# Kernel tuning notes

Measured on AMD Instinct MI355X. Metric: run time of the kernel, lower is better.

## Reference

```python
import jax, jax.numpy as jnp
import numpy as np

B, S = 1, 1536
D_MODEL, NHEAD, HEAD_DIM = 1024, 16, 64
ROPE, NUM_SEQ = 32, 4
KVC, QC, D_FF = 256, 384, 4096
SPP = S // NUM_SEQ                      # seq per stock = 384
EPS_RMS = 1.1920929e-07                 # torch RMSNorm default eps = finfo(fp32).eps
ATTN_EPS = 1e-5
LAMBDA_INIT = 0.8 - 0.6 * float(np.exp(-0.3 * 0.0))  # depth 0 -> 0.2
SCALING = float(((HEAD_DIM + ROPE) // 2) ** -0.5)


def rmsnorm(x, w, eps=EPS_RMS):
    var = jnp.mean(jnp.square(x), axis=-1, keepdims=True)
    return x * jax.lax.rsqrt(var + eps) * w


def setup_inputs() -> dict:
    key = jax.random.key(0)
    ks = jax.random.split(key, 16)
    sd = 0.02
    inv_freq = 1.0 / (10000.0 ** (np.arange(0, ROPE // 4) / (ROPE // 4)))
    ang = np.arange(1, SPP)[:, None] * inv_freq[None, :]  # [SPP-1, ROPE//4]
    return {
        "x": jax.random.normal(ks[0], (B, S, D_MODEL), jnp.float32),
        "freqs_cos": jnp.asarray(np.cos(ang), jnp.float32),
        "freqs_sin": jnp.asarray(np.sin(ang), jnp.float32),
        "norm1_w": jnp.ones((D_MODEL,), jnp.float32),
        "norm2_w": jnp.ones((D_MODEL,), jnp.float32),
        "kv_down_w": jax.random.normal(ks[1], (KVC + ROPE, D_MODEL), jnp.float32) * sd,
        "q_down_w": jax.random.normal(ks[2], (QC, D_MODEL), jnp.float32) * sd,
        "kv_norm_w": jnp.ones((KVC,), jnp.float32),
        "q_norm_w": jnp.ones((QC,), jnp.float32),
        "kv_up_w": jax.random.normal(ks[3], (HEAD_DIM * NHEAD * 2, KVC), jnp.float32) * sd,
        "q_up_w": jax.random.normal(ks[4], ((HEAD_DIM + ROPE) * NHEAD, QC), jnp.float32) * sd,
        "lambda_q1": jax.random.normal(ks[5], (HEAD_DIM // 2,), jnp.float32) * 0.1,
        "lambda_k1": jax.random.normal(ks[6], (HEAD_DIM // 2,), jnp.float32) * 0.1,
        "lambda_q2": jax.random.normal(ks[7], (HEAD_DIM // 2,), jnp.float32) * 0.1,
        "lambda_k2": jax.random.normal(ks[8], (HEAD_DIM // 2,), jnp.float32) * 0.1,
        "attn_norm_w": jnp.ones((HEAD_DIM,), jnp.float32),
        "o_w": jax.random.normal(ks[9], (D_MODEL, NHEAD * HEAD_DIM), jnp.float32) * sd,
        "ff_in_w": jax.random.normal(ks[10], (D_FF * 2, D_MODEL), jnp.float32) * sd,
        "ff_out_w": jax.random.normal(ks[11], (D_MODEL, D_FF), jnp.float32) * sd,
    }


def reference(x, freqs_cos, freqs_sin, norm1_w, norm2_w, kv_down_w, q_down_w,
              kv_norm_w, q_norm_w, kv_up_w, q_up_w, lambda_q1, lambda_k1,
              lambda_q2, lambda_k2, attn_norm_w, o_w, ff_in_w, ff_out_w):
    b, s, _ = x.shape
    spp = s // NUM_SEQ
    H2, hd2 = 2 * NHEAD, HEAD_DIM // 2

    # block-tiled causal mask (1 = masked), matching mask.repeat(..., num_seq, num_seq)
    base = jnp.triu(jnp.ones((spp, spp), jnp.float32), 1)
    mask = jnp.tile(base, (NUM_SEQ, NUM_SEQ))  # [S, S]

    xin = rmsnorm(x, norm1_w)
    ckv = xin @ kv_down_w.T                                    # [B,S,KVC+ROPE]
    c_kv, k_rope = ckv[..., :KVC], ckv[..., KVC:]
    kv = (rmsnorm(c_kv, kv_norm_w) @ kv_up_w.T).reshape(b, s, NHEAD, 2 * HEAD_DIM)
    k, v = kv[..., :HEAD_DIM], kv[..., HEAD_DIM:]
    k = k.reshape(b, s, H2, hd2)
    qf = (rmsnorm(xin @ q_down_w.T, q_norm_w) @ q_up_w.T).reshape(b, s, NHEAD, HEAD_DIM + ROPE)
    q, q_rope = qf[..., :HEAD_DIM], qf[..., HEAD_DIM:]
    q = q.reshape(b, s, H2, hd2)
    k_rope = jnp.tile(k_rope[:, :, None, :], (1, 1, NHEAD, 1)).reshape(b, s, H2, ROPE // 2)
    q_rope = q_rope.reshape(b, s, H2, ROPE // 2)

    # rotary emb; position 0 of every ticker is left untouched (identity rotation)
    cos = jnp.concatenate([jnp.ones((1, ROPE // 4), freqs_cos.dtype), freqs_cos], 0)  # [spp, ROPE//4]
    sin = jnp.concatenate([jnp.zeros((1, ROPE // 4), freqs_sin.dtype), freqs_sin], 0)

    def rot(r):
        # S is laid out as (position, ticker) interleaved: s = p*NUM_SEQ + t
        r = r.reshape(b, spp, NUM_SEQ, H2, ROPE // 4, 2)
        c = cos[None, :, None, None, :]
        s_ = sin[None, :, None, None, :]
        r0, r1 = r[..., 0], r[..., 1]
        y = jnp.stack([r0 * c - r1 * s_, r0 * s_ + r1 * c], axis=-1)
        return y.reshape(b, s, H2, ROPE // 2)

    q = jnp.concatenate([q, rot(q_rope)], -1).transpose(0, 2, 1, 3)  # [B,2H,S,dk]
    k = jnp.concatenate([k, rot(k_rope)], -1).transpose(0, 2, 1, 3)
    v = v.transpose(0, 2, 1, 3)                                      # [B,H,S,hd]

    a = jnp.einsum('bhqd,bhkd->bhqk', q, k) * SCALING
    a = jnp.where(mask[None, None] == 1, -1e9, a)
    a = jax.nn.softmax(a, axis=-1)

    lam = jnp.exp(jnp.sum(lambda_k1 * lambda_q1)) - jnp.exp(jnp.sum(lambda_k2 * lambda_q2)) + LAMBDA_INIT
    a = a.reshape(b, NHEAD, 2, s, s)
    a1, a2 = a[:, :, 0], a[:, :, 1]
    g = jnp.mean(a1, axis=-2, keepdims=True)            # [B,H,1,S], broadcasts over queries
    a = a1 - lam * a2 + lam * g
    a = jnp.where(mask[None, None] == 1, 0.0, a)

    out = jnp.einsum('bhqk,bhkd->bhqd', a, v)           # [B,H,S,hd]
    out = rmsnorm(out.transpose(0, 2, 1, 3), attn_norm_w, eps=ATTN_EPS).transpose(0, 2, 1, 3)
    # faithful to source: raw reshape of [B,H,S,hd] -> [B,S,H*hd] (transposes cancel)
    out = out.reshape(b, s, NHEAD * HEAD_DIM)
    x = x + out @ o_w.T

    h = rmsnorm(x, norm2_w)
    uv = h @ ff_in_w.T
    u, vg = uv[..., :D_FF], uv[..., D_FF:]
    return x + (u * jax.nn.silu(vg)) @ ff_out_w.T
```

## Files before the change

kernel.cpp:

```cpp
#include <hip/hip_runtime.h>
#include <math.h>

#define S     1536
#define DM    1024
#define NH    16
#define H2N   32
#define HD    64
#define KVC   256
#define QC    384
#define DFF   4096
#define SPP   384
#define DQK   48
#define EPS_RMS  1.1920929e-07f
#define ATTN_EPS 1e-5f
#define SCALING  0.14433756729740643f

typedef float f32x4 __attribute__((ext_vector_type(4)));
typedef float f32x16 __attribute__((ext_vector_type(16)));
typedef short bf16x8 __attribute__((ext_vector_type(8)));

__device__ __forceinline__ short cvt_bf16(float f) {
  union { float f; unsigned u; } x; x.f = f;
  unsigned r = x.u + 0x7FFFu + ((x.u >> 16) & 1u);
  return (short)(r >> 16);
}
__device__ __forceinline__ unsigned pk2(float a, float b) {
  unsigned r;
  asm("v_cvt_pk_bf16_f32 %0, %1, %2" : "=v"(r) : "v"(a), "v"(b));
  return r;
}
__device__ __forceinline__ bf16x8 cvt8(float4 a, float4 b) {
  union { unsigned u[4]; bf16x8 v; } r;
  r.u[0] = pk2(a.x, a.y); r.u[1] = pk2(a.z, a.w);
  r.u[2] = pk2(b.x, b.y); r.u[3] = pk2(b.z, b.w);
  return r.v;
}

__global__ __launch_bounds__(256) void cvt_w4(const float* __restrict__ s0, int n0,
    const float* __restrict__ s1, int n1, const float* __restrict__ s2, int n2,
    const float* __restrict__ s3, int n3, short* __restrict__ dst) {
  long base = (long)blockIdx.x * 2048 + (long)threadIdx.x * 8;
  const float* src; long off;
  if (base < n0) { src = s0; off = base; }
  else if (base < (long)n0 + n1) { src = s1; off = base - n0; }
  else if (base < (long)n0 + n1 + n2) { src = s2; off = base - n0 - n1; }
  else { src = s3; off = base - n0 - n1 - n2; }
  float4 a = *reinterpret_cast<const float4*>(src + off);
  float4 b = *reinterpret_cast<const float4*>(src + off + 4);
  *reinterpret_cast<bf16x8*>(dst + base) = cvt8(a, b);
}

__global__ __launch_bounds__(256) void rmsnorm_bf(const float* __restrict__ in,
    const float* __restrict__ w, short* __restrict__ out,
    int cols, int ldin, int ldout, float eps) {
  const int row = blockIdx.x;
  const float* xr = in + (size_t)row * ldin;
  short* yr = out + (size_t)row * ldout;
  const int tid = threadIdx.x;
  float ss = 0.f;
  for (int c = tid << 2; c < cols; c += 1024) {
    float4 v = *reinterpret_cast<const float4*>(xr + c);
    ss += v.x*v.x + v.y*v.y + v.z*v.z + v.w*v.w;
  }
#pragma unroll
  for (int mm = 1; mm < 64; mm <<= 1) ss += __shfl_xor(ss, mm, 64);
  __shared__ float red[4];
  if ((tid & 63) == 0) red[tid >> 6] = ss;
  __syncthreads();
  float tot = red[0] + red[1] + red[2] + red[3];
  float scale = rsqrtf(tot / (float)cols + eps);
  for (int c = tid << 2; c < cols; c += 1024) {
    float4 v = *reinterpret_cast<const float4*>(xr + c);
    float4 wv = *reinterpret_cast<const float4*>(w + c);
    uint2 p;
    p.x = pk2(v.x*scale*wv.x, v.y*scale*wv.y);
    p.y = pk2(v.z*scale*wv.z, v.w*scale*wv.w);
    *reinterpret_cast<uint2*>(yr + c) = p;
  }
}

__global__ __launch_bounds__(256) void rmsnorm_sum_bf(const float* __restrict__ p0,
    const float* __restrict__ p1, const float* __restrict__ xres,
    const float* __restrict__ w, float* __restrict__ outw, short* __restrict__ yb,
    float eps) {
  const int row = blockIdx.x;
  const int c = threadIdx.x << 2;
  const size_t base = (size_t)row * DM + c;
  float4 a = *reinterpret_cast<const float4*>(p0 + base);
  float4 b = *reinterpret_cast<const float4*>(p1 + base);
  float4 xv = *reinterpret_cast<const float4*>(xres + base);
  float4 v = make_float4(a.x+b.x+xv.x, a.y+b.y+xv.y, a.z+b.z+xv.z, a.w+b.w+xv.w);
  *reinterpret_cast<float4*>(outw + base) = v;
  float ss = v.x*v.x + v.y*v.y + v.z*v.z + v.w*v.w;
#pragma unroll
  for (int mm = 1; mm < 64; mm <<= 1) ss += __shfl_xor(ss, mm, 64);
  __shared__ float red[4];
  if ((threadIdx.x & 63) == 0) red[threadIdx.x >> 6] = ss;
  __syncthreads();
  float tot = red[0] + red[1] + red[2] + red[3];
  float scale = rsqrtf(tot * (1.0f / (float)DM) + eps);
  float4 wv = *reinterpret_cast<const float4*>(w + c);
  uint2 p;
  p.x = pk2(v.x*scale*wv.x, v.y*scale*wv.y);
  p.y = pk2(v.z*scale*wv.z, v.w*scale*wv.w);
  *reinterpret_cast<uint2*>(yb + base) = p;
}

__global__ __launch_bounds__(256) void fadd2(float* __restrict__ out,
    const float* __restrict__ p0, const float* __restrict__ p1) {
  size_t i = ((size_t)blockIdx.x * 256 + threadIdx.x) << 2;
  float4 o = *reinterpret_cast<float4*>(out + i);
  float4 a = *reinterpret_cast<const float4*>(p0 + i);
  float4 b = *reinterpret_cast<const float4*>(p1 + i);
  o.x += a.x + b.x; o.y += a.y + b.y; o.z += a.z + b.z; o.w += a.w + b.w;
  *reinterpret_cast<float4*>(out + i) = o;
}

template<int ADD>
__global__ __launch_bounds__(256) void mgemm_nt(const short* __restrict__ A,
    const short* __restrict__ B, const float* __restrict__ src, float* __restrict__ C,
    int M, int N, int K, int lda, int ldb, int ldc) {
  __shared__ short As[64][72];
  __shared__ short Bs[64][72];
  const int bm = blockIdx.y * 64, bn = blockIdx.x * 64;
  const int tid = threadIdx.x;
  const int w = tid >> 6, lane = tid & 63;
  const int wr = (w >> 1) << 5, wc = (w & 1) << 5;
  const int srow = tid >> 2, sk = (tid & 3) << 4;
  const int lrow = lane & 15, lk8 = (lane >> 4) << 3;
  const int arow = bm + srow, brow = bn + srow;
  const bool bvalid = brow < N;
  f32x4 acc[2][2];
#pragma unroll
  for (int i = 0; i < 2; ++i)
#pragma unroll
    for (int j = 0; j < 2; ++j) acc[i][j] = (f32x4){0.f, 0.f, 0.f, 0.f};

  bf16x8 rah0, rah1, rbh0, rbh1;
  {
    const short* ap = A + (size_t)arow * lda + sk;
    rah0 = *reinterpret_cast<const bf16x8*>(ap);
    rah1 = *reinterpret_cast<const bf16x8*>(ap + 8);
  }
  rbh0 = (bf16x8){0,0,0,0,0,0,0,0}; rbh1 = rbh0;
  if (bvalid) {
    const short* bp = B + (size_t)brow * ldb + sk;
    rbh0 = *reinterpret_cast<const bf16x8*>(bp);
    rbh1 = *reinterpret_cast<const bf16x8*>(bp + 8);
  }

  for (int k0 = 0; k0 < K; k0 += 64) {
    bf16x8 va0 = rah0, va1 = rah1, vb0 = rbh0, vb1 = rbh1;
    __syncthreads();
    *reinterpret_cast<bf16x8*>(&As[srow][sk])     = va0;
    *reinterpret_cast<bf16x8*>(&As[srow][sk + 8]) = va1;
    *reinterpret_cast<bf16x8*>(&Bs[srow][sk])     = vb0;
    *reinterpret_cast<bf16x8*>(&Bs[srow][sk + 8]) = vb1;
    __syncthreads();
    const int kn = k0 + 64;
    if (kn < K) {
      const short* ap = A + (size_t)arow * lda + kn + sk;
      rah0 = *reinterpret_cast<const bf16x8*>(ap);
      rah1 = *reinterpret_cast<const bf16x8*>(ap + 8);
      if (bvalid) {
        const short* bp = B + (size_t)brow * ldb + kn + sk;
        rbh0 = *reinterpret_cast<const bf16x8*>(bp);
        rbh1 = *reinterpret_cast<const bf16x8*>(bp + 8);
      }
    }
#pragma unroll
    for (int kk = 0; kk < 2; ++kk) {
      bf16x8 af0 = *reinterpret_cast<bf16x8*>(&As[wr + lrow][(kk << 5) + lk8]);
      bf16x8 af1 = *reinterpret_cast<bf16x8*>(&As[wr + 16 + lrow][(kk << 5) + lk8]);
      bf16x8 bf0 = *reinterpret_cast<bf16x8*>(&Bs[wc + lrow][(kk << 5) + lk8]);
      bf16x8 bf1 = *reinterpret_cast<bf16x8*>(&Bs[wc + 16 + lrow][(kk << 5) + lk8]);
      acc[0][0] = __builtin_amdgcn_mfma_f32_16x16x32_bf16(af0, bf0, acc[0][0], 0, 0, 0);
      acc[0][1] = __builtin_amdgcn_mfma_f32_16x16x32_bf16(af0, bf1, acc[0][1], 0, 0, 0);
      acc[1][0] = __builtin_amdgcn_mfma_f32_16x16x32_bf16(af1, bf0, acc[1][0], 0, 0, 0);
      acc[1][1] = __builtin_amdgcn_mfma_f32_16x16x32_bf16(af1, bf1, acc[1][1], 0, 0, 0);
    }
  }
  const int crow0 = bm + wr + ((lane >> 4) << 2);
  const int ccol0 = bn + wc + lrow;
#pragma unroll
  for (int mi = 0; mi < 2; ++mi)
#pragma unroll
    for (int ni = 0; ni < 2; ++ni) {
      int colc = ccol0 + (ni << 4);
      if (colc < N) {
#pragma unroll
        for (int r = 0; r < 4; ++r) {
          int rowc = crow0 + (mi << 4) + r;
          float v = acc[mi][ni][r];
          if (ADD) v += src[(size_t)rowc * ldc + colc];
          C[(size_t)rowc * ldc + colc] = v;
        }
      }
    }
}

__global__ __launch_bounds__(256) void mgemm_sk(const short* __restrict__ A,
    const short* __restrict__ B, float* __restrict__ P0, float* __restrict__ P1,
    int M, int N, int K2, int lda, int ldb, int ldc) {
  __shared__ short As[64][72];
  __shared__ short Bs[64][72];
  const int bm = blockIdx.y * 64, bn = blockIdx.x * 64;
  const int koff = blockIdx.z * K2;
  float* C = blockIdx.z ? P1 : P0;
  const int tid = threadIdx.x;
  const int w = tid >> 6, lane = tid & 63;
  const int wr = (w >> 1) << 5, wc = (w & 1) << 5;
  const int srow = tid >> 2, sk = (tid & 3) << 4;
  const int lrow = lane & 15, lk8 = (lane >> 4) << 3;
  const int arow = bm + srow, brow = bn + srow;
  f32x4 acc[2][2];
#pragma unroll
  for (int i = 0; i < 2; ++i)
#pragma unroll
    for (int j = 0; j < 2; ++j) acc[i][j] = (f32x4){0.f, 0.f, 0.f, 0.f};

  bf16x8 rah0, rah1, rbh0, rbh1;
  {
    const short* ap = A + (size_t)arow * lda + koff + sk;
    rah0 = *reinterpret_cast<const bf16x8*>(ap);
    rah1 = *reinterpret_cast<const bf16x8*>(ap + 8);
    const short* bp = B + (size_t)brow * ldb + koff + sk;
    rbh0 = *reinterpret_cast<const bf16x8*>(bp);
    rbh1 = *reinterpret_cast<const bf16x8*>(bp + 8);
  }
  const int kend = koff + K2;
  for (int k0 = koff; k0 < kend; k0 += 64) {
    bf16x8 va0 = rah0, va1 = rah1, vb0 = rbh0, vb1 = rbh1;
    __syncthreads();
    *reinterpret_cast<bf16x8*>(&As[srow][sk])     = va0;
    *reinterpret_cast<bf16x8*>(&As[srow][sk + 8]) = va1;
    *reinterpret_cast<bf16x8*>(&Bs[srow][sk])     = vb0;
    *reinterpret_cast<bf16x8*>(&Bs[srow][sk + 8]) = vb1;
    __syncthreads();
    const int kn = k0 + 64;
    if (kn < kend) {
      const short* ap = A + (size_t)arow * lda + kn + sk;
      rah0 = *reinterpret_cast<const bf16x8*>(ap);
      rah1 = *reinterpret_cast<const bf16x8*>(ap + 8);
      const short* bp = B + (size_t)brow * ldb + kn + sk;
      rbh0 = *reinterpret_cast<const bf16x8*>(bp);
      rbh1 = *reinterpret_cast<const bf16x8*>(bp + 8);
    }
#pragma unroll
    for (int kk = 0; kk < 2; ++kk) {
      bf16x8 af0 = *reinterpret_cast<bf16x8*>(&As[wr + lrow][(kk << 5) + lk8]);
      bf16x8 af1 = *reinterpret_cast<bf16x8*>(&As[wr + 16 + lrow][(kk << 5) + lk8]);
      bf16x8 bf0 = *reinterpret_cast<bf16x8*>(&Bs[wc + lrow][(kk << 5) + lk8]);
      bf16x8 bf1 = *reinterpret_cast<bf16x8*>(&Bs[wc + 16 + lrow][(kk << 5) + lk8]);
      acc[0][0] = __builtin_amdgcn_mfma_f32_16x16x32_bf16(af0, bf0, acc[0][0], 0, 0, 0);
      acc[0][1] = __builtin_amdgcn_mfma_f32_16x16x32_bf16(af0, bf1, acc[0][1], 0, 0, 0);
      acc[1][0] = __builtin_amdgcn_mfma_f32_16x16x32_bf16(af1, bf0, acc[1][0], 0, 0, 0);
      acc[1][1] = __builtin_amdgcn_mfma_f32_16x16x32_bf16(af1, bf1, acc[1][1], 0, 0, 0);
    }
  }
  const int crow0 = bm + wr + ((lane >> 4) << 2);
  const int ccol0 = bn + wc + lrow;
#pragma unroll
  for (int mi = 0; mi < 2; ++mi)
#pragma unroll
    for (int ni = 0; ni < 2; ++ni) {
      int colc = ccol0 + (ni << 4);
#pragma unroll
      for (int r = 0; r < 4; ++r) {
        int rowc = crow0 + (mi << 4) + r;
        C[(size_t)rowc * ldc + colc] = acc[mi][ni][r];
      }
    }
}

__global__ __launch_bounds__(256) void mgemm_glu(const short* __restrict__ A,
    const short* __restrict__ Bw, short* __restrict__ C,
    int M, int N, int K, int lda, int ldb, int ldc) {
  __shared__ short As[128][72];
  __shared__ short Bu[64][72];
  __shared__ short Bv[64][72];
  const int bm = blockIdx.y * 128, bn = blockIdx.x * 64;
  const int tid = threadIdx.x;
  const int w = tid >> 6, lane = tid & 63;
  const int wr = (w >> 1) << 6, wc = (w & 1) << 5;
  const int arow = bm + (tid >> 1), ac = (tid & 1) << 5;
  const int brow = bn + (tid >> 2), bc = (tid & 3) << 4;
  const int lrow = lane & 15, lk8 = (lane >> 4) << 3;
  f32x4 au[4][2], av[4][2];
#pragma unroll
  for (int i = 0; i < 4; ++i)
#pragma unroll
    for (int j = 0; j < 2; ++j) {
      au[i][j] = (f32x4){0.f, 0.f, 0.f, 0.f};
      av[i][j] = (f32x4){0.f, 0.f, 0.f, 0.f};
    }
  bf16x8 ra[4], ru[2], rv[2];
  {
    const short* ap = A + (size_t)arow * lda + ac;
    const short* up = Bw + (size_t)brow * ldb + bc;
    const short* vp = Bw + (size_t)(N + brow) * ldb + bc;
#pragma unroll
    for (int e = 0; e < 4; ++e) ra[e] = *reinterpret_cast<const bf16x8*>(ap + (e << 3));
    ru[0] = *reinterpret_cast<const bf16x8*>(up);
    ru[1] = *reinterpret_cast<const bf16x8*>(up + 8);
    rv[0] = *reinterpret_cast<const bf16x8*>(vp);
    rv[1] = *reinterpret_cast<const bf16x8*>(vp + 8);
  }
  for (int k0 = 0; k0 < K; k0 += 64) {
    __syncthreads();
#pragma unroll
    for (int e = 0; e < 4; ++e)
      *reinterpret_cast<bf16x8*>(&As[tid >> 1][ac + (e << 3)]) = ra[e];
    *reinterpret_cast<bf16x8*>(&Bu[tid >> 2][bc])     = ru[0];
    *reinterpret_cast<bf16x8*>(&Bu[tid >> 2][bc + 8]) = ru[1];
    *reinterpret_cast<bf16x8*>(&Bv[tid >> 2][bc])     = rv[0];
    *reinterpret_cast<bf16x8*>(&Bv[tid >> 2][bc + 8]) = rv[1];
    __syncthreads();
    const int kn = k0 + 64;
    if (kn < K) {
      const short* ap = A + (size_t)arow * lda + kn + ac;
      const short* up = Bw + (size_t)brow * ldb + kn + bc;
      const short* vp = Bw + (size_t)(N + brow) * ldb + kn + bc;
#pragma unroll
      for (int e = 0; e < 4; ++e) ra[e] = *reinterpret_cast<const bf16x8*>(ap + (e << 3));
      ru[0] = *reinterpret_cast<const bf16x8*>(up);
      ru[1] = *reinterpret_cast<const bf16x8*>(up + 8);
      rv[0] = *reinterpret_cast<const bf16x8*>(vp);
      rv[1] = *reinterpret_cast<const bf16x8*>(vp + 8);
    }
#pragma unroll
    for (int kk = 0; kk < 2; ++kk) {
      bf16x8 af[4], uf[2], vf[2];
#pragma unroll
      for (int i = 0; i < 4; ++i)
        af[i] = *reinterpret_cast<bf16x8*>(&As[wr + (i << 4) + lrow][(kk << 5) + lk8]);
#pragma unroll
      for (int j = 0; j < 2; ++j) {
        uf[j] = *reinterpret_cast<bf16x8*>(&Bu[wc + (j << 4) + lrow][(kk << 5) + lk8]);
        vf[j] = *reinterpret_cast<bf16x8*>(&Bv[wc + (j << 4) + lrow][(kk << 5) + lk8]);
      }
#pragma unroll
      for (int i = 0; i < 4; ++i)
#pragma unroll
        for (int j = 0; j < 2; ++j) {
          au[i][j] = __builtin_amdgcn_mfma_f32_16x16x32_bf16(af[i], uf[j], au[i][j], 0, 0, 0);
          av[i][j] = __builtin_amdgcn_mfma_f32_16x16x32_bf16(af[i], vf[j], av[i][j], 0, 0, 0);
        }
    }
  }
  const int crow0 = bm + wr + ((lane >> 4) << 2);
  const int ccol0 = bn + wc + lrow;
#pragma unroll
  for (int mi = 0; mi < 4; ++mi)
#pragma unroll
    for (int ni = 0; ni < 2; ++ni) {
      int colc = ccol0 + (ni << 4);
#pragma unroll
      for (int r = 0; r < 4; ++r) {
        int rowc = crow0 + (mi << 4) + r;
        float uu = au[mi][ni][r], vg = av[mi][ni][r];
        float sig = 1.0f / (1.0f + __expf(-vg));
        C[(size_t)rowc * ldc + colc] = cvt_bf16(uu * vg * sig);
      }
    }
}

__global__ __launch_bounds__(256) void build_qk(const float* __restrict__ qf,
    const float* __restrict__ kvb, const float* __restrict__ ckv,
    const float* __restrict__ fc, const float* __restrict__ fs,
    short* __restrict__ Qb, short* __restrict__ Kb) {
  int t = blockIdx.x * 256 + threadIdx.x;
  int h2 = blockIdx.y;
  if (t >= S) return;
  int hh = h2 >> 1, par = h2 & 1;
  const float* qrow = qf + (size_t)t*1536 + hh*96;
  const float* krow = kvb + (size_t)t*2048 + hh*128;
  unsigned qu[24], ku[24];
#pragma unroll
  for (int xq = 0; xq < 8; ++xq) {
    float4 qv = *reinterpret_cast<const float4*>(qrow + par*32 + (xq<<2));
    float4 kv = *reinterpret_cast<const float4*>(krow + par*32 + (xq<<2));
    qu[xq*2]   = pk2(qv.x, qv.y); qu[xq*2+1] = pk2(qv.z, qv.w);
    ku[xq*2]   = pk2(kv.x, kv.y); ku[xq*2+1] = pk2(kv.z, kv.w);
  }
  int p = t >> 2;
  const float* qr = qrow + 64 + par*16;
  const float* kr = ckv + (size_t)t*288 + 256 + par*16;
#pragma unroll
  for (int mq = 0; mq < 8; ++mq) {
    float c = 1.f, sn = 0.f;
    if (p > 0) { c = fc[(p-1)*8 + mq]; sn = fs[(p-1)*8 + mq]; }
    float q0 = qr[2*mq], q1 = qr[2*mq+1];
    qu[16 + mq] = pk2(q0*c - q1*sn, q0*sn + q1*c);
    float k0 = kr[2*mq], k1 = kr[2*mq+1];
    ku[16 + mq] = pk2(k0*c - k1*sn, k0*sn + k1*c);
  }
  unsigned* qo = (unsigned*)(Qb + ((size_t)h2*S + t)*DQK);
  unsigned* ko = (unsigned*)(Kb + ((size_t)h2*S + t)*DQK);
#pragma unroll
  for (int e = 0; e < 6; ++e) {
    *reinterpret_cast<uint4*>(qo + (e<<2)) = make_uint4(qu[e*4], qu[e*4+1], qu[e*4+2], qu[e*4+3]);
    *reinterpret_cast<uint4*>(ko + (e<<2)) = make_uint4(ku[e*4], ku[e*4+1], ku[e*4+2], ku[e*4+3]);
  }
}

__global__ __launch_bounds__(256) void vt_build(const float* __restrict__ kvb,
    short* __restrict__ Vt) {
  const int hh = blockIdx.x;
  const int t0 = blockIdx.y << 7;
  __shared__ short Ts[128][74];
  const int tl = threadIdx.x >> 3, dp = (threadIdx.x & 7) << 3;
#pragma unroll
  for (int pass = 0; pass < 4; ++pass) {
    int t = t0 + (pass << 5) + tl;
    const float* vp = kvb + (size_t)t*2048 + hh*128 + 64 + dp;
    float4 a = *reinterpret_cast<const float4*>(vp);
    float4 b = *reinterpret_cast<const float4*>(vp + 4);
    *reinterpret_cast<bf16x8*>(&Ts[(pass << 5) + tl][dp]) = cvt8(a, b);
  }
  __syncthreads();
  for (int idx = threadIdx.x; idx < 1024; idx += 256) {
    int d = idx >> 4, tseg = (idx & 15) << 3;
    bf16x8 v;
#pragma unroll
    for (int e = 0; e < 8; ++e) v[e] = Ts[tseg + e][d];
    *reinterpret_cast<bf16x8*>(Vt + ((size_t)hh*HD + d)*S + t0 + tseg) = v;
  }
}

__global__ void compute_lam(const float* __restrict__ lq1, const float* __restrict__ lk1,
                            const float* __restrict__ lq2, const float* __restrict__ lk2,
                            float* __restrict__ lamp) {
  int t = threadIdx.x;
  float a = lq1[t]*lk1[t];
  float b = lq2[t]*lk2[t];
#pragma unroll
  for (int mm = 1; mm < 32; mm <<= 1) { a += __shfl_xor(a, mm, 32); b += __shfl_xor(b, mm, 32); }
  if (t == 0) lamp[0] = expf(a) - expf(b) + 0.2f;
}

__global__ __launch_bounds__(256) void flash_mfma(const short* __restrict__ Qb,
    const short* __restrict__ Kb, const short* __restrict__ Vg,
    float* __restrict__ Ob, float* __restrict__ rowm, float* __restrict__ rowl,
    float* __restrict__ Ob1a, float* __restrict__ Ob1b,
    float* __restrict__ rm1, float* __restrict__ rl1) {
  const int h2 = blockIdx.y;
  const int hh = h2 >> 1;
  const int z  = blockIdx.z;
  const int tid = threadIdx.x;
  const int w = tid >> 6, lane = tid & 63;
  const int ql = lane & 31, h = lane >> 5;
  const int cq = blockIdx.x / 3, k = blockIdx.x % 3;
  const int qi = k + 3*w;
  const int qbase = cq*SPP + (qi << 5);
  const int ri0w = qi << 5;

  __shared__ __align__(16) float Ot[4][32][36];

  bf16x8 qf0, qf1, qf2;
  {
    const short* qp = Qb + ((size_t)h2*S + qbase + ql)*DQK + (h << 3);
    qf0 = *reinterpret_cast<const bf16x8*>(qp);
    qf1 = *reinterpret_cast<const bf16x8*>(qp + 16);
    qf2 = *reinterpret_cast<const bf16x8*>(qp + 32);
  }
  const short* Kbase = Kb + (size_t)h2*S*DQK + (h << 3);
  const short* V0 = Vg + ((size_t)hh*HD + ql)*S + (h << 3);
  const short* V1 = Vg + ((size_t)hh*HD + 32 + ql)*S + (h << 3);

  float m = -1e30f, l = 0.f;
  f32x16 o0, o1;
#pragma unroll
  for (int r = 0; r < 16; ++r) { o0[r] = 0.f; o1[r] = 0.f; }

  for (int c = (z << 1); c < (z << 1) + 2; ++c) {
    for (int jr = 0; jr <= ri0w; jr += 32) {
      const int j0 = c*SPP + jr;
      const bool diag = (jr == ri0w);
      const short* kp = Kbase + (size_t)(j0 + ql)*DQK;
      bf16x8 kf0 = *reinterpret_cast<const bf16x8*>(kp);
      bf16x8 kf1 = *reinterpret_cast<const bf16x8*>(kp + 16);
      bf16x8 kf2 = *reinterpret_cast<const bf16x8*>(kp + 32);
      bf16x8 v00 = *reinterpret_cast<const bf16x8*>(V0 + j0);
      bf16x8 v01 = *reinterpret_cast<const bf16x8*>(V0 + j0 + 16);
      bf16x8 v10 = *reinterpret_cast<const bf16x8*>(V1 + j0);
      bf16x8 v11 = *reinterpret_cast<const bf16x8*>(V1 + j0 + 16);

      f32x16 st;
#pragma unroll
      for (int r = 0; r < 16; ++r) st[r] = 0.f;
      st = __builtin_amdgcn_mfma_f32_32x32x16_bf16(kf0, qf0, st, 0, 0, 0);
      st = __builtin_amdgcn_mfma_f32_32x32x16_bf16(kf1, qf1, st, 0, 0, 0);
      st = __builtin_amdgcn_mfma_f32_32x32x16_bf16(kf2, qf2, st, 0, 0, 0);

      if (diag) {
#pragma unroll
        for (int r = 0; r < 16; ++r) {
          int kl = (r & 3) + ((r >> 2) << 3) + (h << 2);
          st[r] = (kl <= ql) ? st[r] * SCALING : -1e30f;
        }
      } else {
#pragma unroll
        for (int r = 0; r < 16; ++r) st[r] *= SCALING;
      }

      float tm = st[0];
#pragma unroll
      for (int r = 1; r < 16; ++r) tm = fmaxf(tm, st[r]);
      tm = fmaxf(tm, __shfl_xor(tm, 32));
      if (__any(tm > m + 8.0f)) {
        float mnew = fmaxf(m, tm);
        float sc = __expf(m - mnew);
        m = mnew;
        l *= sc;
#pragma unroll
        for (int r = 0; r < 16; ++r) { o0[r] *= sc; o1[r] *= sc; }
      }
      float ps = 0.f;
#pragma unroll
      for (int r = 0; r < 16; ++r) { float p = __expf(st[r] - m); st[r] = p; ps += p; }
      ps += __shfl_xor(ps, 32);
      l += ps;

      unsigned A0 = pk2(st[0],  st[1]),  B0 = pk2(st[2],  st[3]);
      unsigned C0 = pk2(st[4],  st[5]),  D0 = pk2(st[6],  st[7]);
      unsigned A1 = pk2(st[8],  st[9]),  B1 = pk2(st[10], st[11]);
      unsigned C1 = pk2(st[12], st[13]), D1 = pk2(st[14], st[15]);
      unsigned xA0 = (unsigned)__shfl_xor((int)A0, 32), xB0 = (unsigned)__shfl_xor((int)B0, 32);
      unsigned xC0 = (unsigned)__shfl_xor((int)C0, 32), xD0 = (unsigned)__shfl_xor((int)D0, 32);
      unsigned xA1 = (unsigned)__shfl_xor((int)A1, 32), xB1 = (unsigned)__shfl_xor((int)B1, 32);
      unsigned xC1 = (unsigned)__shfl_xor((int)C1, 32), xD1 = (unsigned)__shfl_xor((int)D1, 32);
      union { unsigned u[4]; bf16x8 v; } P0, P1;
      P0.u[0] = h ? xC0 : A0;  P0.u[1] = h ? xD0 : B0;
      P0.u[2] = h ? C0 : xA0;  P0.u[3] = h ? D0 : xB0;
      P1.u[0] = h ? xC1 : A1;  P1.u[1] = h ? xD1 : B1;
      P1.u[2] = h ? C1 : xA1;  P1.u[3] = h ? D1 : xB1;

      o0 = __builtin_amdgcn_mfma_f32_32x32x16_bf16(v00, P0.v, o0, 0, 0, 0);
      o0 = __builtin_amdgcn_mfma_f32_32x32x16_bf16(v01, P1.v, o0, 0, 0, 0);
      o1 = __builtin_amdgcn_mfma_f32_32x32x16_bf16(v10, P0.v, o1, 0, 0, 0);
      o1 = __builtin_amdgcn_mfma_f32_32x32x16_bf16(v11, P1.v, o1, 0, 0, 0);
    }
  }

  float* ot = &Ot[w][0][0];
  float* orow;
  if (z == 0) orow = Ob + ((size_t)h2*S + qbase)*HD;
  else orow = (h2 < 16) ? Ob1a + ((size_t)h2*S + qbase)*HD
                        : Ob1b + ((size_t)(h2 - 16)*S + qbase)*HD;
#pragma unroll
  for (int r = 0; r < 16; ++r) {
    int dl = (r & 3) + ((r >> 2) << 3) + (h << 2);
    ot[ql*36 + dl] = o0[r];
  }
#pragma unroll
  for (int it = 0; it < 4; ++it) {
    int idx = lane + (it << 6);
    int row = idx >> 3, c4 = (idx & 7) << 2;
    float4 v = *reinterpret_cast<float4*>(&ot[row*36 + c4]);
    *reinterpret_cast<float4*>(&orow[(size_t)row*HD + c4]) = v;
  }
#pragma unroll
  for (int r = 0; r < 16; ++r) {
    int dl = (r & 3) + ((r >> 2) << 3) + (h << 2);
    ot[ql*36 + dl] = o1[r];
  }
#pragma unroll
  for (int it = 0; it < 4; ++it) {
    int idx = lane + (it << 6);
    int row = idx >> 3, c4 = (idx & 7) << 2;
    float4 v = *reinterpret_cast<float4*>(&ot[row*36 + c4]);
    *reinterpret_cast<float4*>(&orow[(size_t)row*HD + 32 + c4]) = v;
  }
  if (lane < 32) {
    if (z == 0) { rowm[h2*S + qbase + lane] = m; rowl[h2*S + qbase + lane] = l; }
    else        { rm1[h2*S + qbase + lane] = m;  rl1[h2*S + qbase + lane] = l; }
  }
}

__global__ __launch_bounds__(256) void merge_flash(float* __restrict__ Ob,
    float* __restrict__ rowm, float* __restrict__ rowl,
    const float* __restrict__ Ob1a, const float* __restrict__ Ob1b,
    const float* __restrict__ rm1, const float* __restrict__ rl1) {
  const int gid = blockIdx.x * 4 + (threadIdx.x >> 6);
  const int d = threadIdx.x & 63;
  const int h2 = gid / S;
  float m0 = rowm[gid], l0 = rowl[gid], m1 = rm1[gid], l1 = rl1[gid];
  float m = fmaxf(m0, m1);
  float w0 = __expf(m0 - m), w1 = __expf(m1 - m);
  float linv = 1.0f / (l0*w0 + l1*w1);
  const float* o1 = (h2 < 16) ? (Ob1a + (size_t)gid*HD)
                              : (Ob1b + ((size_t)gid - (size_t)16*S)*HD);
  float v0 = Ob[(size_t)gid*HD + d];
  float v1 = o1[d];
  Ob[(size_t)gid*HD + d] = (v0*w0 + v1*w1) * linv;
  if (d == 0) { rowm[gid] = m; rowl[gid] = l0*w0 + l1*w1; }
}

__global__ __launch_bounds__(256) void colsum_mfma(const short* __restrict__ Qb,
    const short* __restrict__ Kb, const float* __restrict__ rowm,
    const float* __restrict__ rowl, float* __restrict__ gcol) {
  const int jt = blockIdx.x;
  const int hh = blockIdx.y, h2 = hh << 1;
  const int cK = jt / 12, jr32 = jt % 12;
  const int jr = jr32 << 5;
  const int j0 = cK*SPP + jr;
  const int tid = threadIdx.x;
  const int w = tid >> 6, lane = tid & 63;
  const int ql = lane & 31, h = lane >> 5;

  bf16x8 kf0, kf1, kf2;
  {
    const short* kp = Kb + ((size_t)h2*S + j0 + ql)*DQK + (h << 3);
    kf0 = *reinterpret_cast<const bf16x8*>(kp);
    kf1 = *reinterpret_cast<const bf16x8*>(kp + 16);
    kf2 = *reinterpret_cast<const bf16x8*>(kp + 32);
  }
  const int nt = 12 - jr32;
  const int T = nt << 2;
  float gs[16];
#pragma unroll
  for (int r = 0; r < 16; ++r) gs[r] = 0.f;

  for (int tt = w; tt < T; tt += 4) {
    int cq = tt / nt, qrem = tt - cq*nt;
    int qi = jr32 + qrem;
    int i0 = cq*SPP + (qi << 5);
    const bool diag = (qrem == 0);
    const short* qp = Qb + ((size_t)h2*S + i0 + ql)*DQK + (h << 3);
    bf16x8 qf0 = *reinterpret_cast<const bf16x8*>(qp);
    bf16x8 qf1 = *reinterpret_cast<const bf16x8*>(qp + 16);
    bf16x8 qf2 = *reinterpret_cast<const bf16x8*>(qp + 32);
    f32x16 st;
#pragma unroll
    for (int r = 0; r < 16; ++r) st[r] = 0.f;
    st = __builtin_amdgcn_mfma_f32_32x32x16_bf16(kf0, qf0, st, 0, 0, 0);
    st = __builtin_amdgcn_mfma_f32_32x32x16_bf16(kf1, qf1, st, 0, 0, 0);
    st = __builtin_amdgcn_mfma_f32_32x32x16_bf16(kf2, qf2, st, 0, 0, 0);
    float Mq = rowm[h2*S + i0 + ql];
    float Lq = 1.0f / rowl[h2*S + i0 + ql];
    if (diag) {
#pragma unroll
      for (int r = 0; r < 16; ++r) {
        int kl = (r & 3) + ((r >> 2) << 3) + (h << 2);
        if (kl <= ql) gs[r] += __expf(st[r]*SCALING - Mq) * Lq;
      }
    } else {
#pragma unroll
      for (int r = 0; r < 16; ++r) gs[r] += __expf(st[r]*SCALING - Mq) * Lq;
    }
  }
  __shared__ float gw[4][32];
#pragma unroll
  for (int r = 0; r < 16; ++r) {
    float v = gs[r];
#pragma unroll
    for (int mm = 1; mm < 32; mm <<= 1) v += __shfl_xor(v, mm, 32);
    if (ql == 0) gw[w][(r & 3) + ((r >> 2) << 3) + (h << 2)] = v;
  }
  __syncthreads();
  if (tid < 32) {
    float s = gw[0][tid] + gw[1][tid] + gw[2][tid] + gw[3][tid];
    gcol[hh*S + j0 + tid] = s * (1.0f / (float)S);
  }
}

__global__ __launch_bounds__(256) void build_wpre(const float* __restrict__ gcol,
    const float* __restrict__ kvb, float* __restrict__ Wpre) {
  const int hh = blockIdx.x >> 2;
  const int dq = (blockIdx.x & 3) << 4;
  __shared__ float Wt[SPP][16];
  const int tid = threadIdx.x;
  for (int idx = tid; idx < SPP*16; idx += 256) {
    int r = idx >> 4, dd = idx & 15;
    float val = 0.f;
#pragma unroll
    for (int b2 = 0; b2 < 4; ++b2) {
      int j = b2*SPP + r;
      val = fmaf(gcol[hh*S + j], kvb[(size_t)j*2048 + hh*128 + 64 + dq + dd], val);
    }
    Wt[r][dd] = val;
  }
  __syncthreads();
  if (tid < 16) {
    float run = 0.f;
    for (int r = 0; r < SPP; ++r) { run += Wt[r][tid]; Wt[r][tid] = run; }
  }
  __syncthreads();
  for (int idx = tid; idx < SPP*16; idx += 256) {
    int r = idx >> 4, dd = idx & 15;
    Wpre[((size_t)hh*SPP + r)*HD + dq + dd] = Wt[r][dd];
  }
}

__global__ __launch_bounds__(64) void combine_rms(const float* __restrict__ Ob,
    const float* __restrict__ Wpre, const float* __restrict__ lamp,
    const float* __restrict__ anw, short* __restrict__ attno) {
  const int t = blockIdx.x, h = blockIdx.y, d = threadIdx.x;
  const float lam = lamp[0];
  const float o1 = Ob[((size_t)(2*h)*S + t)*HD + d];
  const float o2 = Ob[((size_t)(2*h+1)*S + t)*HD + d];
  const float w3 = Wpre[((size_t)h*SPP + (t % SPP))*HD + d];
  float val = o1 - lam*o2 + lam*w3;
  float ss = val*val;
#pragma unroll
  for (int mm = 1; mm < 64; mm <<= 1) ss += __shfl_xor(ss, mm, 64);
  float scale = rsqrtf(ss * (1.0f/HD) + ATTN_EPS) * anw[d];
  int tn = h*96 + (t >> 4);
  int cn = ((t & 15) << 6) + d;
  attno[(size_t)tn*DM + cn] = cvt_bf16(val * scale);
}

extern "C" void kernel_launch(void* const* d_in, const int* in_sizes, int n_in,
                              void* d_out, int out_size, void* d_ws, size_t ws_size,
                              hipStream_t stream) {
  (void)in_sizes; (void)n_in; (void)out_size;
  const float* x    = (const float*)d_in[0];
  const float* fc   = (const float*)d_in[1];
  const float* fs   = (const float*)d_in[2];
  const float* n1w  = (const float*)d_in[3];
  const float* n2w  = (const float*)d_in[4];
  const float* kvdw = (const float*)d_in[5];
  const float* qdw  = (const float*)d_in[6];
  const float* kvnw = (const float*)d_in[7];
  const float* qnw  = (const float*)d_in[8];
  const float* kvuw = (const float*)d_in[9];
  const float* quw  = (const float*)d_in[10];
  const float* lq1  = (const float*)d_in[11];
  const float* lk1  = (const float*)d_in[12];
  const float* lq2  = (const float*)d_in[13];
  const float* lk2  = (const float*)d_in[14];
  const float* anw  = (const float*)d_in[15];
  const float* ow   = (const float*)d_in[16];
  const float* ffiw = (const float*)d_in[17];
  const float* ffow = (const float*)d_in[18];
  float* out = (float*)d_out;
  float* ws  = (float*)d_ws;

  float* xin   = ws;
  float* ckv   = xin   + (size_t)S*DM;
  float* qmid  = ckv   + (size_t)S*288;
  float* kvb   = qmid  + (size_t)S*QC;
  float* qf    = kvb   + (size_t)S*2048;
  float* Qb    = qf    + (size_t)S*1536;
  float* Kb    = Qb    + (size_t)H2N*S*DQK;
  float* Obuf  = Kb    + (size_t)H2N*S*DQK;
  float* rowm  = Obuf  + (size_t)H2N*S*HD;
  float* rowl  = rowm  + (size_t)H2N*S;
  float* gcol  = rowl  + (size_t)H2N*S;
  float* Wpre  = gcol  + (size_t)NH*S;
  float* attno = Wpre  + (size_t)NH*SPP*HD;
  float* lamp  = attno + (size_t)S*DM;
  short* fbufs = (short*)kvb;
  float* Ob1a = xin;
  float* Ob1b = qf;
  float* rm1  = qf + (size_t)16*S*HD;
  float* rl1  = rm1 + (size_t)H2N*S;
  short* Qb_bf = (short*)Qb;
  short* Kb_bf = (short*)Kb;
  short* Vt_bf = (short*)Qb + 2359296;
  short* xin_bf  = (short*)xin;
  short* ckv_bf  = (short*)Obuf;
  short* qmid_bf = ckv_bf + (size_t)S*KVC;
  short* h_bf    = (short*)ckv;
  short* attno_bf = (short*)attno;
  short* kvdw_bf = (short*)attno;
  short* qdw_bf  = kvdw_bf + 294912;
  short* kvuw_bf = qdw_bf  + 393216;
  short* quw_bf  = kvuw_bf + 524288;
  short* ffiw_bf = (short*)Qb;
  short* ow_bf   = ffiw_bf + 8388608;
  short* ffow_bf = (short*)Obuf;
  float* psum0 = xin;
  float* psum1 = qf;
  if (ws_size < (size_t)18063376 * sizeof(float)) return;

  cvt_w4<<<880, 256, 0, stream>>>(kvdw, 294912, qdw, 393216, kvuw, 524288, quw, 589824, kvdw_bf);
  rmsnorm_bf<<<S, 256, 0, stream>>>(x, n1w, xin_bf, DM, DM, DM, EPS_RMS);
  { dim3 g(5, 24);  mgemm_nt<0><<<g, 256, 0, stream>>>(xin_bf, kvdw_bf, nullptr, ckv, S, 288, DM, DM, DM, 288); }
  { dim3 g(6, 24);  mgemm_nt<0><<<g, 256, 0, stream>>>(xin_bf, qdw_bf,  nullptr, qmid, S, QC, DM, DM, DM, QC); }
  rmsnorm_bf<<<S, 256, 0, stream>>>(ckv,  kvnw, ckv_bf,  KVC, 288, KVC, EPS_RMS);
  rmsnorm_bf<<<S, 256, 0, stream>>>(qmid, qnw,  qmid_bf, QC,  QC,  QC,  EPS_RMS);
  { dim3 g(32, 24); mgemm_nt<0><<<g, 256, 0, stream>>>(ckv_bf,  kvuw_bf, nullptr, kvb, S, 2048, KVC, KVC, KVC, 2048); }
  { dim3 g(24, 24); mgemm_nt<0><<<g, 256, 0, stream>>>(qmid_bf, quw_bf,  nullptr, qf,  S, 1536, QC,  QC,  QC,  1536); }
  { dim3 g(6, 32);  build_qk<<<g, 256, 0, stream>>>(qf, kvb, ckv, fc, fs, Qb_bf, Kb_bf); }
  { dim3 g(16, 12); vt_build<<<g, 256, 0, stream>>>(kvb, Vt_bf); }
  compute_lam<<<1, 32, 0, stream>>>(lq1, lk1, lq2, lk2, lamp);
  { dim3 g(12, 32, 2); flash_mfma<<<g, 256, 0, stream>>>(Qb_bf, Kb_bf, Vt_bf, Obuf, rowm, rowl,
                                                         Ob1a, Ob1b, rm1, rl1); }
  merge_flash<<<(H2N*S)/4, 256, 0, stream>>>(Obuf, rowm, rowl, Ob1a, Ob1b, rm1, rl1);
  { dim3 g(48, 16); colsum_mfma<<<g, 256, 0, stream>>>(Qb_bf, Kb_bf, rowm, rowl, gcol); }
  cvt_w4<<<4608, 256, 0, stream>>>(ffiw, 8388608, ow, 1048576, nullptr, 0, nullptr, 0, ffiw_bf);
  build_wpre<<<64, 256, 0, stream>>>(gcol, kvb, Wpre);
  { dim3 g(S, 16);  combine_rms<<<g, 64, 0, stream>>>(Obuf, Wpre, lamp, anw, attno_bf); }
  cvt_w4<<<2048, 256, 0, stream>>>(ffow, 4194304, nullptr, 0, nullptr, 0, nullptr, 0, ffow_bf);
  { dim3 g(16, 24, 2); mgemm_sk<<<g, 256, 0, stream>>>(attno_bf, ow_bf, psum0, psum1, S, DM, 512, DM, DM, DM); }
  rmsnorm_sum_bf<<<S, 256, 0, stream>>>(psum0, psum1, x, n2w, out, h_bf, EPS_RMS);
  { dim3 g(64, 12); mgemm_glu<<<g, 256, 0, stream>>>(h_bf, ffiw_bf, fbufs, S, DFF, DM, DM, DM, DFF); }
  { dim3 g(16, 24, 2); mgemm_sk<<<g, 256, 0, stream>>>(fbufs, ffow_bf, psum0, psum1, S, DM, 2048, DFF, DFF, DM); }
  fadd2<<<1536, 256, 0, stream>>>(out, psum0, psum1);
}
```

Measured before the change: 235.9 us.

## Fuse KV/Q down-projections into one GEMM, merge their RMSNorms, swizzle GEMM tiles

Concatenates the kv_down and q_down weights, which are already contiguous in the bf16 buffer, so one GEMM produces a 672-wide output instead of two launches. A new two-segment RMSNorm kernel replaces the two separate norm launches, and build_qk now reads the rope part with the new row stride. Separately, all GEMM kernels remap block indices with an 8-way swizzle so that neighbouring workgroups are spread across XCDs. This removes launch overhead and improves occupancy for the small GEMMs, but the 672-column output is not a multiple of 64, so the last tile column is partial and relies on the N bounds check.

```diff
diff --git a/kernel.cpp b/kernel.cpp
--- a/kernel.cpp
+++ b/kernel.cpp
@@ -11,6 +11,7 @@
 #define DFF   4096
 #define SPP   384
 #define DQK   48
+#define CKW   672
 #define EPS_RMS  1.1920929e-07f
 #define ATTN_EPS 1e-5f
 #define SCALING  0.14433756729740643f
@@ -34,6 +35,10 @@
   r.u[0] = pk2(a.x, a.y); r.u[1] = pk2(a.z, a.w);
   r.u[2] = pk2(b.x, b.y); r.u[3] = pk2(b.z, b.w);
   return r.v;
+}
+__device__ __forceinline__ int swz8(int flat, int nwg) {
+  if (nwg & 7) return flat;
+  return (flat & 7) * (nwg >> 3) + (flat >> 3);
 }
 
 __global__ __launch_bounds__(256) void cvt_w4(const float* __restrict__ s0, int n0,
@@ -79,6 +84,38 @@
   }
 }
 
+__global__ __launch_bounds__(256) void rmsnorm2_bf(const float* __restrict__ comb,
+    const float* __restrict__ w0, const float* __restrict__ w1,
+    short* __restrict__ o0, short* __restrict__ o1, float eps) {
+  const int row = blockIdx.x;
+  const int seg = blockIdx.y;
+  const float* xr = comb + (size_t)row * CKW + (seg ? 288 : 0);
+  const float* w  = seg ? w1 : w0;
+  short* yr = seg ? (o1 + (size_t)row * QC) : (o0 + (size_t)row * KVC);
+  const int cols = seg ? QC : KVC;
+  const int tid = threadIdx.x;
+  float ss = 0.f;
+  for (int c = tid << 2; c < cols; c += 1024) {
+    float4 v = *reinterpret_cast<const float4*>(xr + c);
+    ss += v.x*v.x + v.y*v.y + v.z*v.z + v.w*v.w;
+  }
+#pragma unroll
+  for (int mm = 1; mm < 64; mm <<= 1) ss += __shfl_xor(ss, mm, 64);
+  __shared__ float red[4];
+  if ((tid & 63) == 0) red[tid >> 6] = ss;
+  __syncthreads();
+  float tot = red[0] + red[1] + red[2] + red[3];
+  float scale = rsqrtf(tot / (float)cols + eps);
+  for (int c = tid << 2; c < cols; c += 1024) {
+    float4 v = *reinterpret_cast<const float4*>(xr + c);
+    float4 wv = *reinterpret_cast<const float4*>(w + c);
+    uint2 p;
+    p.x = pk2(v.x*scale*wv.x, v.y*scale*wv.y);
+    p.y = pk2(v.z*scale*wv.z, v.w*scale*wv.w);
+    *reinterpret_cast<uint2*>(yr + c) = p;
+  }
+}
+
 __global__ __launch_bounds__(256) void rmsnorm_sum_bf(const float* __restrict__ p0,
     const float* __restrict__ p1, const float* __restrict__ xres,
     const float* __restrict__ w, float* __restrict__ outw, short* __restrict__ yb,
@@ -122,7 +159,10 @@
     int M, int N, int K, int lda, int ldb, int ldc) {
   __shared__ short As[64][72];
   __shared__ short Bs[64][72];
-  const int bm = blockIdx.y * 64, bn = blockIdx.x * 64;
+  const int nwg = gridDim.x * gridDim.y;
+  const int sfl = swz8(blockIdx.y * gridDim.x + blockIdx.x, nwg);
+  const int bxs = sfl % gridDim.x, bys = sfl / gridDim.x;
+  const int bm = bys * 64, bn = bxs * 64;
   const int tid = threadIdx.x;
   const int w = tid >> 6, lane = tid & 63;
   const int wr = (w >> 1) << 5, wc = (w & 1) << 5;
@@ -204,7 +244,10 @@
     int M, int N, int K2, int lda, int ldb, int ldc) {
   __shared__ short As[64][72];
   __shared__ short Bs[64][72];
-  const int bm = blockIdx.y * 64, bn = blockIdx.x * 64;
+  const int nwg = gridDim.x * gridDim.y;
+  const int sfl = swz8(blockIdx.y * gridDim.x + blockIdx.x, nwg);
+  const int bxs = sfl % gridDim.x, bys = sfl / gridDim.x;
+  const int bm = bys * 64, bn = bxs * 64;
   const int koff = blockIdx.z * K2;
   float* C = blockIdx.z ? P1 : P0;
   const int tid = threadIdx.x;
@@ -279,7 +322,10 @@
   __shared__ short As[128][72];
   __shared__ short Bu[64][72];
   __shared__ short Bv[64][72];
-  const int bm = blockIdx.y * 128, bn = blockIdx.x * 64;
+  const int nwg = gridDim.x * gridDim.y;
+  const int sfl = swz8(blockIdx.y * gridDim.x + blockIdx.x, nwg);
+  const int bxs = sfl % gridDim.x, bys = sfl / gridDim.x;
+  const int bm = bys * 128, bn = bxs * 64;
   const int tid = threadIdx.x;
   const int w = tid >> 6, lane = tid & 63;
   const int wr = (w >> 1) << 6, wc = (w & 1) << 5;
@@ -385,7 +431,7 @@
   }
   int p = t >> 2;
   const float* qr = qrow + 64 + par*16;
-  const float* kr = ckv + (size_t)t*288 + 256 + par*16;
+  const float* kr = ckv + (size_t)t*CKW + 256 + par*16;
 #pragma unroll
   for (int mq = 0; mq < 8; ++mq) {
     float c = 1.f, sn = 0.f;
@@ -777,10 +823,8 @@
 
   cvt_w4<<<880, 256, 0, stream>>>(kvdw, 294912, qdw, 393216, kvuw, 524288, quw, 589824, kvdw_bf);
   rmsnorm_bf<<<S, 256, 0, stream>>>(x, n1w, xin_bf, DM, DM, DM, EPS_RMS);
-  { dim3 g(5, 24);  mgemm_nt<0><<<g, 256, 0, stream>>>(xin_bf, kvdw_bf, nullptr, ckv, S, 288, DM, DM, DM, 288); }
-  { dim3 g(6, 24);  mgemm_nt<0><<<g, 256, 0, stream>>>(xin_bf, qdw_bf,  nullptr, qmid, S, QC, DM, DM, DM, QC); }
-  rmsnorm_bf<<<S, 256, 0, stream>>>(ckv,  kvnw, ckv_bf,  KVC, 288, KVC, EPS_RMS);
-  rmsnorm_bf<<<S, 256, 0, stream>>>(qmid, qnw,  qmid_bf, QC,  QC,  QC,  EPS_RMS);
+  { dim3 g(11, 24); mgemm_nt<0><<<g, 256, 0, stream>>>(xin_bf, kvdw_bf, nullptr, ckv, S, CKW, DM, DM, DM, CKW); }
+  { dim3 g(S, 2);   rmsnorm2_bf<<<g, 256, 0, stream>>>(ckv, kvnw, qnw, ckv_bf, qmid_bf, EPS_RMS); }
   { dim3 g(32, 24); mgemm_nt<0><<<g, 256, 0, stream>>>(ckv_bf,  kvuw_bf, nullptr, kvb, S, 2048, KVC, KVC, KVC, 2048); }
   { dim3 g(24, 24); mgemm_nt<0><<<g, 256, 0, stream>>>(qmid_bf, quw_bf,  nullptr, qf,  S, 1536, QC,  QC,  QC,  1536); }
   { dim3 g(6, 32);  build_qk<<<g, 256, 0, stream>>>(qf, kvb, ckv, fc, fs, Qb_bf, Kb_bf); }
```

After: 225.7 us. 4.3% less time.
